# Kernel optimization log

Measured on AMD Instinct MI355X. Metric: run time of the kernel, lower is better.

The kernel has to match this reference:

```python
import jax, jax.numpy as jnp
import numpy as np

N_NODES = 50000
N_EDGES = 500000
NUM_FEAT = 128
NUM_CLASSES = 112
HID = 18
HEADS = 8
OUT_DIM = 144  # hidden_dim * heads = 18*8 = 144, also final GAT out_dim
N_GRAPHS = 64
EPS = 1e-5
NEG_SLOPE = 0.2


def setup_inputs() -> dict:
    key = jax.random.key(0)
    ks = jax.random.split(key, 32)
    f32 = jnp.float32
    def rn(k, shape, scale=0.1):
        return jax.random.normal(k, shape, f32) * scale
    x = jax.random.normal(ks[0], (N_NODES, NUM_FEAT), f32)
    edge_index = jax.random.randint(ks[1], (2, N_EDGES), 0, N_NODES)
    batch = jnp.sort(jax.random.randint(ks[2], (N_NODES,), 0, N_GRAPHS))
    D = HID * HEADS  # 144
    params = dict(
        x=x, edge_index=edge_index, batch=batch,
        We=rn(ks[3], (NUM_FEAT, D)), be=jnp.zeros((D,), f32),
        Wg=rn(ks[4], (3, D, D)),
        a_sg=rn(ks[5], (3, HEADS, HID)), a_dg=rn(ks[6], (3, HEADS, HID)),
        bg=jnp.zeros((3, D), f32),
        gam=jnp.ones((3, D), f32), bet=jnp.zeros((3, D), f32),
        W3=rn(ks[7], (D, OUT_DIM)),
        a_s3=rn(ks[8], (1, OUT_DIM)), a_d3=rn(ks[9], (1, OUT_DIM)),
        b3=jnp.zeros((OUT_DIM,), f32),
        gam3=jnp.ones((OUT_DIM,), f32), bet3=jnp.zeros((OUT_DIM,), f32),
        M1=rn(ks[10], (OUT_DIM, 72)), bm1=jnp.zeros((72,), f32),
        gm1=jnp.ones((72,), f32), bb1=jnp.zeros((72,), f32),
        M2=rn(ks[11], (72, 36)), bm2=jnp.zeros((36,), f32),
        gm2=jnp.ones((36,), f32), bb2=jnp.zeros((36,), f32),
        M3=rn(ks[12], (36, NUM_CLASSES)), bm3=jnp.zeros((NUM_CLASSES,), f32),
    )
    return params


def _gat_layer(h, src, dst, W, a_s, a_d, b, heads, out_ch):
    # PyG GATConv: per-head linear, additive attention, segment softmax over dst
    N = h.shape[0]
    hp = (h @ W).reshape(N, heads, out_ch)                 # [N,H,C]
    al_s = (hp * a_s).sum(-1)                              # [N,H]
    al_d = (hp * a_d).sum(-1)                              # [N,H]
    e = jax.nn.leaky_relu(al_s[src] + al_d[dst], NEG_SLOPE)  # [E,H]
    m = jax.ops.segment_max(e, dst, num_segments=N)
    ex = jnp.exp(e - m[dst])
    den = jax.ops.segment_sum(ex, dst, num_segments=N)
    alpha = ex / (den[dst] + 1e-16)                        # [E,H]
    out = jax.ops.segment_sum(hp[src] * alpha[..., None], dst, num_segments=N)
    return out.reshape(N, heads * out_ch) + b


def _bn(x, g, b):
    mu = x.mean(0)
    v = jnp.var(x, axis=0)
    return g * (x - mu) * jax.lax.rsqrt(v + EPS) + b


def reference(x, edge_index, batch, We, be, Wg, a_sg, a_dg, bg, gam, bet,
              W3, a_s3, a_d3, b3, gam3, bet3,
              M1, bm1, gm1, bb1, M2, bm2, gm2, bb2, M3, bm3):
    N = x.shape[0]
    loops = jnp.arange(N)  # GATConv add_self_loops=True
    src = jnp.concatenate([edge_index[0], loops])
    dst = jnp.concatenate([edge_index[1], loops])
    out = x @ We + be
    for i in range(3):
        out = _gat_layer(out, src, dst, Wg[i], a_sg[i], a_dg[i], bg[i], HEADS, HID)
        out = jax.nn.relu(out)
        out = _bn(out, gam[i], bet[i])
    out = _gat_layer(out, src, dst, W3, a_s3, a_d3, b3, 1, OUT_DIM)
    out = jax.nn.relu(out)
    out = _bn(out, gam3, bet3)
    # global mean pool over graphs
    sums = jax.ops.segment_sum(out, batch, num_segments=N_GRAPHS)
    cnt = jax.ops.segment_sum(jnp.ones((N, 1), out.dtype), batch, num_segments=N_GRAPHS)
    g = sums / jnp.maximum(cnt, 1.0)
    # PyG MLP: lin -> batchnorm -> relu (plain last layer)
    h = jax.nn.relu(_bn(g @ M1 + bm1, gm1, bb1))
    h = jax.nn.relu(_bn(h @ M2 + bm2, gm2, bb2))
    return h @ M3 + bm3
```

## Files before the change

kernel.cpp:

```cpp
#include <hip/hip_runtime.h>
#include <cstdint>

#define N_NODESC 50000
#define N_EDGESC 500000
#define E_TOT    550000
#define DIM      144
#define NGRAPH   64
#define EPSV     1e-5f
#define SCAN_NB  ((N_NODESC + 511)/512)

typedef __attribute__((ext_vector_type(8))) short bf16x8;
typedef __attribute__((ext_vector_type(4))) float f32x4;

__device__ __forceinline__ float lrelu(float x){ return x > 0.f ? x : 0.2f*x; }

__device__ __forceinline__ unsigned short f2bf(float f){
  unsigned u = __float_as_uint(f);
  u += 0x7FFF + ((u >> 16) & 1);
  return (unsigned short)(u >> 16);
}
__device__ __forceinline__ float bf2f(unsigned short b){
  return __uint_as_float(((unsigned)b) << 16);
}

__global__ void k_count(const int* __restrict__ ei, int* __restrict__ deg){
  int e = blockIdx.x*blockDim.x + threadIdx.x;
  if (e >= E_TOT) return;
  int d = (e < N_EDGESC) ? ei[N_EDGESC + e] : (e - N_EDGESC);
  atomicAdd(&deg[d], 1);
}

__global__ __launch_bounds__(256) void k_scan1(const int* __restrict__ deg,
    int* __restrict__ scanned, int* __restrict__ bsum){
  __shared__ int ls[256];
  int b = blockIdx.x, t = threadIdx.x;
  int i0 = b*512 + 2*t;
  int e0 = (i0   < N_NODESC) ? deg[i0]   : 0;
  int e1 = (i0+1 < N_NODESC) ? deg[i0+1] : 0;
  int s = e0 + e1;
  ls[t] = s;
  __syncthreads();
  #pragma unroll
  for (int ofs=1; ofs<256; ofs<<=1){
    int v = (t >= ofs) ? ls[t-ofs] : 0;
    __syncthreads();
    ls[t] += v;
    __syncthreads();
  }
  int excl = ls[t] - s;
  if (i0   < N_NODESC) scanned[i0]   = excl;
  if (i0+1 < N_NODESC) scanned[i0+1] = excl + e0;
  if (t == 255) bsum[b] = ls[255];
}

__global__ void k_scan2(int* __restrict__ bsum){
  __shared__ int ls[128];
  int t = threadIdx.x;
  int v = (t < SCAN_NB) ? bsum[t] : 0;
  ls[t] = v;
  __syncthreads();
  #pragma unroll
  for (int ofs=1; ofs<128; ofs<<=1){
    int u = (t >= ofs) ? ls[t-ofs] : 0;
    __syncthreads();
    ls[t] += u;
    __syncthreads();
  }
  if (t < SCAN_NB) bsum[t] = ls[t] - v;
}

__global__ __launch_bounds__(256) void k_scan3(const int* __restrict__ scanned,
    const int* __restrict__ bsum, int* __restrict__ row_ptr, int* __restrict__ cursor){
  int i = blockIdx.x*blockDim.x + threadIdx.x;
  if (i < N_NODESC){
    int v = scanned[i] + bsum[i >> 9];
    row_ptr[i] = v; cursor[i] = v;
  }
  if (i == 0) row_ptr[N_NODESC] = E_TOT;
}

__global__ void k_scatter(const int* __restrict__ ei, int* __restrict__ cursor,
                          int* __restrict__ col){
  int e = blockIdx.x*blockDim.x + threadIdx.x;
  if (e >= E_TOT) return;
  int s, d;
  if (e < N_EDGESC){ s = ei[e]; d = ei[N_EDGESC + e]; } else { s = e - N_EDGESC; d = s; }
  int pos = atomicAdd(&cursor[d], 1);
  col[pos] = s;
}

__global__ void k_cast(const float* __restrict__ x, unsigned short* __restrict__ xb){
  int i = blockIdx.x*blockDim.x + threadIdx.x;
  if (i < N_NODESC*128) xb[i] = f2bf(x[i]);
}

__global__ __launch_bounds__(192) void k_prep_w(
    const float* __restrict__ W, const float* __restrict__ bias_in,
    const float* __restrict__ a_s, const float* __restrict__ a_d,
    const float* __restrict__ bnsum, const float* __restrict__ bngam,
    const float* __restrict__ bnbet,
    unsigned short* __restrict__ Wt, float* __restrict__ bias2,
    int K, int SK, int H){
  __shared__ float red[256];
  int np = blockIdx.x, k = threadIdx.x;
  float sc = 1.f, sh = 0.f;
  if (k < K && bnsum){
    float mu  = bnsum[k] * (1.f/N_NODESC);
    float var = bnsum[K+k] * (1.f/N_NODESC) - mu*mu;
    float inv = rsqrtf(var + EPSV);
    sc = inv * bngam[k];
    sh = bnbet[k] - mu*sc;
  }
  float wcomb = 0.f;
  if (k < K){
    if (np < 144) wcomb = W[(size_t)k*144 + np];
    else if (H > 0){
      int c = np - 144;
      bool iss = c < 8;
      int h = iss ? c : c - 8;
      if (h < H){
        const float* av = iss ? a_s : a_d;
        int C = 144 / H;
        for (int j=0;j<C;++j) wcomb += W[(size_t)k*144 + h*C + j] * av[h*C + j];
      }
    }
  }
  if (k < SK) Wt[(size_t)np*SK + k] = f2bf(wcomb*sc);
  red[k] = (k < K) ? sh*wcomb : 0.f;
  if (k < 64) red[k+192] = 0.f;
  __syncthreads();
  #pragma unroll
  for (int s=128; s>0; s>>=1){
    if (k < s) red[k] += red[k+s];
    __syncthreads();
  }
  if (k == 0){
    float b = red[0];
    if (np < 144 && bias_in) b += bias_in[np];
    bias2[np] = b;
  }
}

template<int NT, int KS, int SK, int NROW>
__global__ __launch_bounds__(256) void k_mfma_gemm(
    const unsigned short* __restrict__ A,
    const unsigned short* __restrict__ Wt,
    const float* __restrict__ bias2,
    unsigned short* __restrict__ hp,
    float* __restrict__ al_s, float* __restrict__ al_d,
    int KA, int H){
  __shared__ unsigned short sW[NROW*SK];
  int t = threadIdx.x;
  for (int i = t; i < NROW*SK/8; i += 256)
    ((uint4*)sW)[i] = ((const uint4*)Wt)[i];
  __syncthreads();

  int wave = t >> 6, lane = t & 63;
  int c = lane & 15, quad = lane >> 4;
  int m_base = blockIdx.x*64 + wave*16;
  int mA = m_base + c; if (mA > N_NODESC-1) mA = N_NODESC-1;
  f32x4 acc[NT];
  #pragma unroll
  for (int i=0;i<NT;++i) acc[i] = (f32x4){0.f,0.f,0.f,0.f};
  const unsigned short* Arow = A + (size_t)mA*KA + quad*8;
  #pragma unroll
  for (int ks=0; ks<KS; ++ks){
    bf16x8 af = *(const bf16x8*)(Arow + ks*32);
    #pragma unroll
    for (int tt=0; tt<NT; ++tt){
      bf16x8 bfr = *(const bf16x8*)(sW + (tt*16 + c)*SK + ks*32 + quad*8);
      acc[tt] = __builtin_amdgcn_mfma_f32_16x16x32_bf16(af, bfr, acc[tt], 0, 0, 0);
    }
  }
  #pragma unroll
  for (int tt=0; tt<NT; ++tt){
    int n = tt*16 + c;
    float b = bias2[n];
    #pragma unroll
    for (int r=0;r<4;++r){
      int m = m_base + quad*4 + r;
      if (m < N_NODESC){
        float v = acc[tt][r] + b;
        if (n < 144){
          hp[(size_t)m*144 + n] = f2bf(v);
        } else {
          int cc = n - 144;
          if (cc < 8){ if (cc < H) al_s[m*H + cc] = v; }
          else { int h = cc - 8; if (h < H) al_d[m*H + h] = v; }
        }
      }
    }
  }
}

#define EB 8
__global__ __launch_bounds__(256) void k_edge_softmax(
    const float* __restrict__ al_s, const float* __restrict__ al_d,
    const int* __restrict__ row_ptr, const int* __restrict__ col,
    float* __restrict__ esc, float* __restrict__ den, int H){
  int idx = blockIdx.x*blockDim.x + threadIdx.x;
  if (idx >= N_NODESC*H) return;
  int n = idx / H, h = idx - n*H;
  int p0 = row_ptr[n], p1 = row_ptr[n+1];
  float ald = al_d[idx];
  float m = -3.4e38f, d = 0.f;
  for (int base = p0; base < p1; base += EB){
    int cnt = min(EB, p1 - base);
    int ss[EB];
    #pragma unroll
    for (int i=0;i<EB;++i) if (i<cnt) ss[i] = col[base+i];
    float sc[EB];
    #pragma unroll
    for (int i=0;i<EB;++i) if (i<cnt) sc[i] = lrelu(al_s[ss[i]*H + h] + ald);
    float bm = -3.4e38f;
    #pragma unroll
    for (int i=0;i<EB;++i) if (i<cnt){
      esc[(size_t)(base+i)*H + h] = sc[i];
      bm = fmaxf(bm, sc[i]);
    }
    if (bm > m){ d *= __expf(m - bm); m = bm; }
    #pragma unroll
    for (int i=0;i<EB;++i) if (i<cnt) d += __expf(sc[i] - m);
  }
  den[idx] = d;
  for (int e = p0; e < p1; ++e)
    esc[(size_t)e*H + h] = __expf(esc[(size_t)e*H + h] - m);
}

__global__ __launch_bounds__(256) void k_aggregate2(
    const unsigned* __restrict__ hp2, const float* __restrict__ w,
    const float* __restrict__ den,
    const int* __restrict__ row_ptr, const int* __restrict__ col,
    const float* __restrict__ bias, unsigned* __restrict__ out,
    int H, int C2){
  int idx = blockIdx.x*blockDim.x + threadIdx.x;
  if (idx >= N_NODESC*72) return;
  int n = idx / 72, cp = idx - n*72;
  int h = cp / C2;
  int p0 = row_ptr[n], p1 = row_ptr[n+1];
  float a0 = 0.f, a1 = 0.f;
  for (int base = p0; base < p1; base += EB){
    int cnt = min(EB, p1 - base);
    int ss[EB]; float ww[EB];
    #pragma unroll
    for (int i=0;i<EB;++i) if (i<cnt){
      ss[i] = col[base+i];
      ww[i] = w[(size_t)(base+i)*H + h];
    }
    unsigned vv[EB];
    #pragma unroll
    for (int i=0;i<EB;++i) if (i<cnt) vv[i] = hp2[(size_t)ss[i]*72 + cp];
    #pragma unroll
    for (int i=0;i<EB;++i) if (i<cnt){
      a0 = fmaf(ww[i], __uint_as_float(vv[i] << 16), a0);
      a1 = fmaf(ww[i], __uint_as_float(vv[i] & 0xFFFF0000u), a1);
    }
  }
  float dv = 1.f/(den[n*H + h] + 1e-16f);
  int c0 = 2*cp;
  float r0 = fmaxf(a0*dv + bias[c0],   0.f);
  float r1 = fmaxf(a1*dv + bias[c0+1], 0.f);
  out[(size_t)n*72 + cp] = (unsigned)f2bf(r0) | ((unsigned)f2bf(r1) << 16);
}

#define BNS_GRID 512
__global__ __launch_bounds__(256) void k_bnstats1(const uint2* __restrict__ h4,
                                                  float* __restrict__ partials){
  __shared__ float red[252*8];
  int t = threadIdx.x;
  int r = t / 36, c = t - r*36;
  bool active = (t < 252);
  int rows = (N_NODESC + BNS_GRID - 1)/BNS_GRID;
  int n0 = blockIdx.x*rows, n1 = min(N_NODESC, n0+rows);
  float s[4] = {0,0,0,0}, q[4] = {0,0,0,0};
  if (active){
    for (int n = n0 + r; n < n1; n += 7){
      uint2 v = h4[(size_t)n*36 + c];
      float f0 = __uint_as_float(v.x << 16);
      float f1 = __uint_as_float(v.x & 0xFFFF0000u);
      float f2 = __uint_as_float(v.y << 16);
      float f3 = __uint_as_float(v.y & 0xFFFF0000u);
      s[0]+=f0; q[0]+=f0*f0; s[1]+=f1; q[1]+=f1*f1;
      s[2]+=f2; q[2]+=f2*f2; s[3]+=f3; q[3]+=f3*f3;
    }
    #pragma unroll
    for (int j=0;j<4;++j){
      red[(c*7+r)*8 + j]     = s[j];
      red[(c*7+r)*8 + 4 + j] = q[j];
    }
  }
  __syncthreads();
  if (t < 36){
    float ss[4]={0,0,0,0}, qq[4]={0,0,0,0};
    for (int rr=0; rr<7; ++rr){
      #pragma unroll
      for (int j=0;j<4;++j){
        ss[j] += red[(t*7+rr)*8 + j];
        qq[j] += red[(t*7+rr)*8 + 4 + j];
      }
    }
    float* p = partials + (size_t)blockIdx.x*288;
    #pragma unroll
    for (int j=0;j<4;++j){
      p[4*t+j]       = ss[j];
      p[144+4*t+j]   = qq[j];
    }
  }
}

__global__ __launch_bounds__(64) void k_bnstats2(const float* __restrict__ partials,
                                                 float* __restrict__ sums){
  int i = blockIdx.x, t = threadIdx.x;
  float s = 0.f;
  for (int b = t; b < BNS_GRID; b += 64) s += partials[(size_t)b*288 + i];
  #pragma unroll
  for (int o=32; o>0; o>>=1) s += __shfl_xor(s, o, 64);
  if (t == 0) sums[i] = s;
}

__device__ int lbound(const int* a, int n, int v){
  int lo = 0, hi = n;
  while (lo < hi){ int m = (lo+hi) >> 1; if (a[m] < v) lo = m+1; else hi = m; }
  return lo;
}

__global__ __launch_bounds__(128) void k_pool(const unsigned* __restrict__ h2,
    const int* __restrict__ batch, float* __restrict__ sums, int* __restrict__ cnts){
  int g = blockIdx.x & 63, part = blockIdx.x >> 6;
  __shared__ int sb[2];
  if (threadIdx.x == 0){ sb[0] = lbound(batch, N_NODESC, g); sb[1] = lbound(batch, N_NODESC, g+1); }
  __syncthreads();
  int lo = sb[0], hi = sb[1];
  int t = threadIdx.x;
  if (t < 72){
    float a0 = 0.f, a1 = 0.f;
    for (int n = lo + part; n < hi; n += 32){
      unsigned v = h2[(size_t)n*72 + t];
      a0 += __uint_as_float(v << 16);
      a1 += __uint_as_float(v & 0xFFFF0000u);
    }
    atomicAdd(&sums[g*DIM + 2*t],   a0);
    atomicAdd(&sums[g*DIM + 2*t+1], a1);
  }
  if (t == 0 && part == 0) cnts[g] = hi - lo;
}

__global__ __launch_bounds__(64) void k_mlp1(const float* __restrict__ psum,
    const int* __restrict__ cnts,
    const float* __restrict__ bn3, const float* __restrict__ gam3,
    const float* __restrict__ bet3,
    const float* __restrict__ M1, const float* __restrict__ bm1,
    const float* __restrict__ gm1, const float* __restrict__ bb1,
    float* __restrict__ h1){
  __shared__ float sSc[144], sSh[144];
  int t = threadIdx.x, c = blockIdx.x;
  for (int i=t; i<144; i+=64){
    float mu  = bn3[i] * (1.f/N_NODESC);
    float var = bn3[144+i] * (1.f/N_NODESC) - mu*mu;
    float sc  = rsqrtf(var + EPSV) * gam3[i];
    sSc[i] = sc; sSh[i] = bet3[i] - mu*sc;
  }
  __syncthreads();
  float invc = 1.f / (float)max(cnts[t], 1);
  float acc = bm1[c];
  const float* pr = psum + t*144;
  for (int k=0; k<144; ++k){
    float g = fmaf(pr[k]*invc, sSc[k], sSh[k]);
    acc = fmaf(g, M1[k*72 + c], acc);
  }
  float s = acc, q = acc*acc;
  #pragma unroll
  for (int o=32; o>0; o>>=1){ s += __shfl_xor(s, o, 64); q += __shfl_xor(q, o, 64); }
  float mu = s*(1.f/64.f), var = q*(1.f/64.f) - mu*mu;
  float v = (acc - mu)*rsqrtf(var + EPSV)*gm1[c] + bb1[c];
  h1[t*72 + c] = fmaxf(v, 0.f);
}

__global__ __launch_bounds__(64) void k_mlp2(const float* __restrict__ h1,
    const float* __restrict__ M2, const float* __restrict__ bm2,
    const float* __restrict__ gm2, const float* __restrict__ bb2,
    float* __restrict__ h2){
  int t = threadIdx.x, c = blockIdx.x;
  float acc = bm2[c];
  const float* pr = h1 + t*72;
  for (int k=0; k<72; ++k) acc = fmaf(pr[k], M2[k*36 + c], acc);
  float s = acc, q = acc*acc;
  #pragma unroll
  for (int o=32; o>0; o>>=1){ s += __shfl_xor(s, o, 64); q += __shfl_xor(q, o, 64); }
  float mu = s*(1.f/64.f), var = q*(1.f/64.f) - mu*mu;
  float v = (acc - mu)*rsqrtf(var + EPSV)*gm2[c] + bb2[c];
  h2[t*36 + c] = fmaxf(v, 0.f);
}

__global__ __launch_bounds__(64) void k_mlp3(const float* __restrict__ h2,
    const float* __restrict__ M3, const float* __restrict__ bm3,
    float* __restrict__ out){
  int t = threadIdx.x, c = blockIdx.x;
  float acc = bm3[c];
  const float* pr = h2 + t*36;
  for (int k=0; k<36; ++k) acc = fmaf(pr[k], M3[k*112 + c], acc);
  out[t*112 + c] = acc;
}

extern "C" void kernel_launch(void* const* d_in, const int* in_sizes, int n_in,
                              void* d_out, int out_size, void* d_ws, size_t ws_size,
                              hipStream_t stream){
  const float* x    = (const float*)d_in[0];
  const int*   ei   = (const int*)d_in[1];
  const int*   batch= (const int*)d_in[2];
  const float* We   = (const float*)d_in[3];
  const float* be   = (const float*)d_in[4];
  const float* Wg   = (const float*)d_in[5];
  const float* a_sg = (const float*)d_in[6];
  const float* a_dg = (const float*)d_in[7];
  const float* bg   = (const float*)d_in[8];
  const float* gam  = (const float*)d_in[9];
  const float* bet  = (const float*)d_in[10];
  const float* W3   = (const float*)d_in[11];
  const float* a_s3 = (const float*)d_in[12];
  const float* a_d3 = (const float*)d_in[13];
  const float* b3   = (const float*)d_in[14];
  const float* gam3 = (const float*)d_in[15];
  const float* bet3 = (const float*)d_in[16];
  const float* M1   = (const float*)d_in[17];
  const float* bm1  = (const float*)d_in[18];
  const float* gm1  = (const float*)d_in[19];
  const float* bb1  = (const float*)d_in[20];
  const float* M2   = (const float*)d_in[21];
  const float* bm2  = (const float*)d_in[22];
  const float* gm2  = (const float*)d_in[23];
  const float* bb2  = (const float*)d_in[24];
  const float* M3   = (const float*)d_in[25];
  const float* bm3  = (const float*)d_in[26];
  float* out = (float*)d_out;

  char* ws = (char*)d_ws;
  size_t off = 0;
  auto alloc = [&](size_t bytes)->char*{
    char* p = ws + off; off += (bytes + 255) & ~(size_t)255; return p;
  };
  unsigned short* hAb = (unsigned short*)alloc((size_t)N_NODESC*DIM*2);
  unsigned short* hp  = (unsigned short*)alloc((size_t)N_NODESC*DIM*2);
  unsigned short* xb  = (unsigned short*)alloc((size_t)N_NODESC*128*2);
  float* al_s   = (float*)alloc((size_t)N_NODESC*8*4);
  float* al_d   = (float*)alloc((size_t)N_NODESC*8*4);
  float* den    = (float*)alloc((size_t)N_NODESC*8*4);
  float* esc    = (float*)alloc((size_t)E_TOT*8*4);
  int* row_ptr  = (int*)alloc((size_t)(N_NODESC+1)*4);
  int* deg      = (int*)alloc((size_t)N_NODESC*4);
  int* cursor   = (int*)alloc((size_t)N_NODESC*4);
  int* scanned  = (int*)alloc((size_t)N_NODESC*4);
  int* bsum     = (int*)alloc((size_t)SCAN_NB*4);
  int* col      = (int*)alloc((size_t)E_TOT*4);
  float* bns4   = (float*)alloc(4*2*DIM*4);
  float* partials = (float*)alloc((size_t)BNS_GRID*288*4);
  float* psum   = (float*)alloc((size_t)NGRAPH*DIM*4);
  int* pcnt     = (int*)alloc(NGRAPH*4);
  float* h1buf  = (float*)alloc((size_t)NGRAPH*72*4);
  float* h2buf  = (float*)alloc((size_t)NGRAPH*36*4);
  unsigned short* Wt = (unsigned short*)alloc((size_t)160*168*2);
  float* bias2  = (float*)alloc(160*4);
  (void)ws_size; (void)n_in; (void)in_sizes; (void)out_size;

  const int GEMM_GRID = (N_NODESC + 63)/64;

  hipMemsetAsync(deg, 0, (size_t)N_NODESC*4, stream);
  k_count<<<(E_TOT+255)/256, 256, 0, stream>>>(ei, deg);
  k_scan1<<<SCAN_NB, 256, 0, stream>>>(deg, scanned, bsum);
  k_scan2<<<1, 128, 0, stream>>>(bsum);
  k_scan3<<<(N_NODESC+255)/256, 256, 0, stream>>>(scanned, bsum, row_ptr, cursor);
  k_scatter<<<(E_TOT+255)/256, 256, 0, stream>>>(ei, cursor, col);

  k_cast<<<(N_NODESC*128+255)/256, 256, 0, stream>>>(x, xb);
  k_prep_w<<<144, 192, 0, stream>>>(We, be, nullptr, nullptr,
                                    nullptr, nullptr, nullptr, Wt, bias2, 128, 136, 0);
  k_mfma_gemm<9,4,136,144><<<GEMM_GRID, 256, 0, stream>>>(
      xb, Wt, bias2, hAb, nullptr, nullptr, 128, 0);

  for (int L=0; L<4; ++L){
    const float* W  = (L<3) ? (Wg  + (size_t)L*DIM*DIM) : W3;
    const float* as = (L<3) ? (a_sg + (size_t)L*8*18)   : a_s3;
    const float* ad = (L<3) ? (a_dg + (size_t)L*8*18)   : a_d3;
    const float* bb = (L<3) ? (bg  + L*DIM) : b3;
    int H = (L<3) ? 8 : 1;
    int C = (L<3) ? 18 : 144;
    const float* bnp = (L==0) ? nullptr : bns4 + (size_t)(L-1)*2*DIM;
    const float* gmp = (L==0) ? nullptr : gam + (size_t)(L-1)*DIM;
    const float* btp = (L==0) ? nullptr : bet + (size_t)(L-1)*DIM;
    k_prep_w<<<160, 192, 0, stream>>>(W, nullptr, as, ad,
                                      bnp, gmp, btp, Wt, bias2, 144, 168, H);
    k_mfma_gemm<10,5,168,160><<<GEMM_GRID, 256, 0, stream>>>(
        hAb, Wt, bias2, hp, al_s, al_d, 144, H);
    k_edge_softmax<<<(N_NODESC*H+255)/256, 256, 0, stream>>>(
        al_s, al_d, row_ptr, col, esc, den, H);
    k_aggregate2<<<(N_NODESC*72+255)/256, 256, 0, stream>>>(
        (const unsigned*)hp, esc, den, row_ptr, col, bb, (unsigned*)hAb, H, C/2);
    k_bnstats1<<<BNS_GRID, 256, 0, stream>>>((const uint2*)hAb, partials);
    k_bnstats2<<<288, 64, 0, stream>>>(partials, bns4 + (size_t)L*2*DIM);
  }

  hipMemsetAsync(psum, 0, (size_t)NGRAPH*DIM*4, stream);
  k_pool<<<NGRAPH*32, 128, 0, stream>>>((const unsigned*)hAb, batch, psum, pcnt);
  k_mlp1<<<72, 64, 0, stream>>>(psum, pcnt, bns4 + 3*2*DIM, gam3, bet3,
                                M1, bm1, gm1, bb1, h1buf);
  k_mlp2<<<36, 64, 0, stream>>>(h1buf, M2, bm2, gm2, bb2, h2buf);
  k_mlp3<<<112, 64, 0, stream>>>(h2buf, M3, bm3, out);
}
```

Baseline: 653.7 us.

## Fuse input cast into GEMM, prenormalize bf16 attention weights, widen aggregation

Removes the separate f32-to-bf16 cast kernel by converting x inside the first MFMA GEMM's A loads. Edge softmax now writes weights already divided by the denominator as bf16, so aggregation no longer reads den and moves half the weight bytes. Aggregation processes four channels per thread with 8-byte gathers, halving thread count and index/weight reloads. The cost is reduced precision of the attention weights, which are now stored in bf16.

```diff
diff --git a/kernel.cpp b/kernel.cpp
--- a/kernel.cpp
+++ b/kernel.cpp
@@ -87,11 +87,6 @@
   if (e < N_EDGESC){ s = ei[e]; d = ei[N_EDGESC + e]; } else { s = e - N_EDGESC; d = s; }
   int pos = atomicAdd(&cursor[d], 1);
   col[pos] = s;
-}
-
-__global__ void k_cast(const float* __restrict__ x, unsigned short* __restrict__ xb){
-  int i = blockIdx.x*blockDim.x + threadIdx.x;
-  if (i < N_NODESC*128) xb[i] = f2bf(x[i]);
 }
 
 __global__ __launch_bounds__(192) void k_prep_w(
@@ -141,9 +136,9 @@
   }
 }
 
-template<int NT, int KS, int SK, int NROW>
+template<int NT, int KS, int SK, int NROW, int AF32>
 __global__ __launch_bounds__(256) void k_mfma_gemm(
-    const unsigned short* __restrict__ A,
+    const void* __restrict__ Av,
     const unsigned short* __restrict__ Wt,
     const float* __restrict__ bias2,
     unsigned short* __restrict__ hp,
@@ -162,10 +157,20 @@
   f32x4 acc[NT];
   #pragma unroll
   for (int i=0;i<NT;++i) acc[i] = (f32x4){0.f,0.f,0.f,0.f};
-  const unsigned short* Arow = A + (size_t)mA*KA + quad*8;
   #pragma unroll
   for (int ks=0; ks<KS; ++ks){
-    bf16x8 af = *(const bf16x8*)(Arow + ks*32);
+    bf16x8 af;
+    if (AF32){
+      const float* Arow = (const float*)Av + (size_t)mA*KA + quad*8;
+      float4 f0 = *(const float4*)(Arow + ks*32);
+      float4 f1 = *(const float4*)(Arow + ks*32 + 4);
+      unsigned short tmp[8] = { f2bf(f0.x),f2bf(f0.y),f2bf(f0.z),f2bf(f0.w),
+                                f2bf(f1.x),f2bf(f1.y),f2bf(f1.z),f2bf(f1.w) };
+      af = *(const bf16x8*)tmp;
+    } else {
+      const unsigned short* Arow = (const unsigned short*)Av + (size_t)mA*KA + quad*8;
+      af = *(const bf16x8*)(Arow + ks*32);
+    }
     #pragma unroll
     for (int tt=0; tt<NT; ++tt){
       bf16x8 bfr = *(const bf16x8*)(sW + (tt*16 + c)*SK + ks*32 + quad*8);
@@ -197,7 +202,7 @@
 __global__ __launch_bounds__(256) void k_edge_softmax(
     const float* __restrict__ al_s, const float* __restrict__ al_d,
     const int* __restrict__ row_ptr, const int* __restrict__ col,
-    float* __restrict__ esc, float* __restrict__ den, int H){
+    float* __restrict__ esc, unsigned short* __restrict__ wN, int H){
   int idx = blockIdx.x*blockDim.x + threadIdx.x;
   if (idx >= N_NODESC*H) return;
   int n = idx / H, h = idx - n*H;
@@ -222,45 +227,51 @@
     #pragma unroll
     for (int i=0;i<EB;++i) if (i<cnt) d += __expf(sc[i] - m);
   }
-  den[idx] = d;
+  float inv = 1.f/(d + 1e-16f);
   for (int e = p0; e < p1; ++e)
-    esc[(size_t)e*H + h] = __expf(esc[(size_t)e*H + h] - m);
+    wN[(size_t)e*H + h] = f2bf(__expf(esc[(size_t)e*H + h] - m) * inv);
 }
 
 __global__ __launch_bounds__(256) void k_aggregate2(
-    const unsigned* __restrict__ hp2, const float* __restrict__ w,
-    const float* __restrict__ den,
+    const uint2* __restrict__ hp4, const unsigned short* __restrict__ wN,
     const int* __restrict__ row_ptr, const int* __restrict__ col,
-    const float* __restrict__ bias, unsigned* __restrict__ out,
+    const float* __restrict__ bias, uint2* __restrict__ out,
     int H, int C2){
   int idx = blockIdx.x*blockDim.x + threadIdx.x;
-  if (idx >= N_NODESC*72) return;
-  int n = idx / 72, cp = idx - n*72;
-  int h = cp / C2;
+  if (idx >= N_NODESC*36) return;
+  int n = idx / 36, cp2 = idx - n*36;
+  int h0 = (2*cp2) / C2, h1 = (2*cp2 + 1) / C2;
   int p0 = row_ptr[n], p1 = row_ptr[n+1];
-  float a0 = 0.f, a1 = 0.f;
+  float a0=0.f, a1=0.f, a2=0.f, a3=0.f;
   for (int base = p0; base < p1; base += EB){
     int cnt = min(EB, p1 - base);
-    int ss[EB]; float ww[EB];
+    int ss[EB]; float w0[EB], w1[EB];
     #pragma unroll
     for (int i=0;i<EB;++i) if (i<cnt){
       ss[i] = col[base+i];
-      ww[i] = w[(size_t)(base+i)*H + h];
-    }
-    unsigned vv[EB];
-    #pragma unroll
-    for (int i=0;i<EB;++i) if (i<cnt) vv[i] = hp2[(size_t)ss[i]*72 + cp];
+      w0[i] = bf2f(wN[(size_t)(base+i)*H + h0]);
+      w1[i] = bf2f(wN[(size_t)(base+i)*H + h1]);
+    }
+    uint2 vv[EB];
+    #pragma unroll
+    for (int i=0;i<EB;++i) if (i<cnt) vv[i] = hp4[(size_t)ss[i]*36 + cp2];
     #pragma unroll
     for (int i=0;i<EB;++i) if (i<cnt){
-      a0 = fmaf(ww[i], __uint_as_float(vv[i] << 16), a0);
-      a1 = fmaf(ww[i], __uint_as_float(vv[i] & 0xFFFF0000u), a1);
-    }
-  }
-  float dv = 1.f/(den[n*H + h] + 1e-16f);
-  int c0 = 2*cp;
-  float r0 = fmaxf(a0*dv + bias[c0],   0.f);
-  float r1 = fmaxf(a1*dv + bias[c0+1], 0.f);
-  out[(size_t)n*72 + cp] = (unsigned)f2bf(r0) | ((unsigned)f2bf(r1) << 16);
+      a0 = fmaf(w0[i], __uint_as_float(vv[i].x << 16), a0);
+      a1 = fmaf(w0[i], __uint_as_float(vv[i].x & 0xFFFF0000u), a1);
+      a2 = fmaf(w1[i], __uint_as_float(vv[i].y << 16), a2);
+      a3 = fmaf(w1[i], __uint_as_float(vv[i].y & 0xFFFF0000u), a3);
+    }
+  }
+  int c0 = 4*cp2;
+  float r0 = fmaxf(a0 + bias[c0],   0.f);
+  float r1 = fmaxf(a1 + bias[c0+1], 0.f);
+  float r2 = fmaxf(a2 + bias[c0+2], 0.f);
+  float r3 = fmaxf(a3 + bias[c0+3], 0.f);
+  uint2 o;
+  o.x = (unsigned)f2bf(r0) | ((unsigned)f2bf(r1) << 16);
+  o.y = (unsigned)f2bf(r2) | ((unsigned)f2bf(r3) << 16);
+  out[(size_t)n*36 + cp2] = o;
 }
 
 #define BNS_GRID 512
@@ -441,11 +452,10 @@
   };
   unsigned short* hAb = (unsigned short*)alloc((size_t)N_NODESC*DIM*2);
   unsigned short* hp  = (unsigned short*)alloc((size_t)N_NODESC*DIM*2);
-  unsigned short* xb  = (unsigned short*)alloc((size_t)N_NODESC*128*2);
   float* al_s   = (float*)alloc((size_t)N_NODESC*8*4);
   float* al_d   = (float*)alloc((size_t)N_NODESC*8*4);
-  float* den    = (float*)alloc((size_t)N_NODESC*8*4);
   float* esc    = (float*)alloc((size_t)E_TOT*8*4);
+  unsigned short* wN = (unsigned short*)alloc((size_t)E_TOT*8*2);
   int* row_ptr  = (int*)alloc((size_t)(N_NODESC+1)*4);
   int* deg      = (int*)alloc((size_t)N_NODESC*4);
   int* cursor   = (int*)alloc((size_t)N_NODESC*4);
@@ -471,11 +481,10 @@
   k_scan3<<<(N_NODESC+255)/256, 256, 0, stream>>>(scanned, bsum, row_ptr, cursor);
   k_scatter<<<(E_TOT+255)/256, 256, 0, stream>>>(ei, cursor, col);
 
-  k_cast<<<(N_NODESC*128+255)/256, 256, 0, stream>>>(x, xb);
   k_prep_w<<<144, 192, 0, stream>>>(We, be, nullptr, nullptr,
                                     nullptr, nullptr, nullptr, Wt, bias2, 128, 136, 0);
-  k_mfma_gemm<9,4,136,144><<<GEMM_GRID, 256, 0, stream>>>(
-      xb, Wt, bias2, hAb, nullptr, nullptr, 128, 0);
+  k_mfma_gemm<9,4,136,144,1><<<GEMM_GRID, 256, 0, stream>>>(
+      x, Wt, bias2, hAb, nullptr, nullptr, 128, 0);
 
   for (int L=0; L<4; ++L){
     const float* W  = (L<3) ? (Wg  + (size_t)L*DIM*DIM) : W3;
@@ -489,12 +498,12 @@
     const float* btp = (L==0) ? nullptr : bet + (size_t)(L-1)*DIM;
     k_prep_w<<<160, 192, 0, stream>>>(W, nullptr, as, ad,
                                       bnp, gmp, btp, Wt, bias2, 144, 168, H);
-    k_mfma_gemm<10,5,168,160><<<GEMM_GRID, 256, 0, stream>>>(
+    k_mfma_gemm<10,5,168,160,0><<<GEMM_GRID, 256, 0, stream>>>(
         hAb, Wt, bias2, hp, al_s, al_d, 144, H);
     k_edge_softmax<<<(N_NODESC*H+255)/256, 256, 0, stream>>>(
-        al_s, al_d, row_ptr, col, esc, den, H);
-    k_aggregate2<<<(N_NODESC*72+255)/256, 256, 0, stream>>>(
-        (const unsigned*)hp, esc, den, row_ptr, col, bb, (unsigned*)hAb, H, C/2);
+        al_s, al_d, row_ptr, col, esc, wN, H);
+    k_aggregate2<<<(N_NODESC*36+255)/256, 256, 0, stream>>>(
+        (const uint2*)hp, wN, row_ptr, col, bb, (uint2*)hAb, H, C/2);
     k_bnstats1<<<BNS_GRID, 256, 0, stream>>>((const uint2*)hAb, partials);
     k_bnstats2<<<288, 64, 0, stream>>>(partials, bns4 + (size_t)L*2*DIM);
   }
```

Result: slower. 682.9 us (+4.5%).
